# Performance work log

Measured on AMD Instinct MI355X. Metric: run time of the kernel, lower is better.

## Reference

```python
import jax, jax.numpy as jnp
import numpy as np

N_TASK = 100_000
N_DATA = 50_000
E = 1_500_000
D_TASK = 64
D_DATA = 64
D_EDGE = 16
H = 2
C = 64


def setup_inputs() -> dict:
    key = jax.random.key(0)
    ks = jax.random.split(key, 16)
    g = lambda k, shape, s=0.05: jax.random.normal(k, shape, jnp.float32) * s
    return {
        "task_x": jax.random.normal(ks[0], (N_TASK, D_TASK), jnp.float32),
        "data_x": jax.random.normal(ks[1], (N_DATA, D_DATA), jnp.float32),
        "edge_attr": jax.random.normal(ks[2], (E, D_EDGE), jnp.float32),
        "src_idx": jax.random.randint(ks[3], (E,), 0, N_DATA),
        "dst_idx": jax.random.randint(ks[4], (E,), 0, N_TASK),
        # GATv2Conv params
        "W_l": g(ks[5], (D_DATA, H * C)),   # lin_l (source/data)
        "b_l": jnp.zeros((H * C,), jnp.float32),
        "W_r": g(ks[6], (D_TASK, H * C)),   # lin_r (dest/tasks)
        "b_r": jnp.zeros((H * C,), jnp.float32),
        "W_e": g(ks[7], (D_EDGE, H * C)),   # lin_edge (no bias)
        "att": g(ks[8], (H, C)),
        "W_res": g(ks[9], (D_TASK, C)),     # residual lin (no bias)
        "conv_bias": jnp.zeros((C,), jnp.float32),
        # LayerNorm params
        "ln_g": jnp.ones((C,), jnp.float32),
        "ln_b": jnp.zeros((C,), jnp.float32),
    }


def reference(task_x, data_x, edge_attr, src_idx, dst_idx,
              W_l, b_l, W_r, b_r, W_e, att, W_res, conv_bias, ln_g, ln_b):
    n_task = task_x.shape[0]
    x_l = (data_x @ W_l + b_l).reshape(-1, H, C)      # [N_data, H, C]
    x_r = (task_x @ W_r + b_r).reshape(-1, H, C)      # [N_task, H, C]
    e = (edge_attr @ W_e).reshape(-1, H, C)           # [E, H, C]

    # GATv2 attention: leaky_relu(x_i + x_j + e) . att, negative_slope=0.2
    x = jax.nn.leaky_relu(x_l[src_idx] + x_r[dst_idx] + e, 0.2)  # [E, H, C]
    alpha = jnp.einsum("ehc,hc->eh", x, att)                      # [E, H]

    # per-destination-node segment softmax
    m = jax.ops.segment_max(alpha, dst_idx, num_segments=n_task)  # [N_task, H]
    m = jnp.where(jnp.isfinite(m), m, 0.0)  # empty segments -> 0
    a = jnp.exp(alpha - m[dst_idx])
    denom = jax.ops.segment_sum(a, dst_idx, num_segments=n_task)
    a = a / (denom[dst_idx] + 1e-16)                              # [E, H]

    # message = lin_l(x_src), weighted and scatter-summed to destinations
    out = jax.ops.segment_sum(x_l[src_idx] * a[..., None], dst_idx,
                              num_segments=n_task)                # [N_task, H, C]
    out = out.mean(axis=1)                                        # concat=False -> head mean
    out = out + task_x @ W_res + conv_bias                        # residual + bias

    # LayerNorm over channels
    mu = out.mean(-1, keepdims=True)
    var = out.var(-1, keepdims=True)
    out = (out - mu) / jnp.sqrt(var + 1e-5) * ln_g + ln_b

    out = jax.nn.leaky_relu(out, 0.01)
    return jnp.concatenate([out, task_x], axis=-1)                # [N_task, C + D_TASK]
```

## Files before the change

### kernel.cpp

```cpp
#include <hip/hip_runtime.h>
#include <hip/hip_bf16.h>

#define N_TASK 100000
#define N_DATA 50000
#define NE     1500000
#define PAD    48

typedef _Float16 half2v __attribute__((ext_vector_type(2)));
typedef float    f32x4  __attribute__((ext_vector_type(4)));
typedef unsigned u32x2  __attribute__((ext_vector_type(2)));
typedef int      i32x2  __attribute__((ext_vector_type(2)));
typedef int      i32x4  __attribute__((ext_vector_type(4)));

__device__ __forceinline__ unsigned pack_f16(float a, float b) {
    half2v h = {(_Float16)a, (_Float16)b};
    return __builtin_bit_cast(unsigned, h);
}
__device__ __forceinline__ float f16_lo(unsigned u) {
    half2v h = __builtin_bit_cast(half2v, u); return (float)h.x;
}
__device__ __forceinline__ float f16_hi(unsigned u) {
    half2v h = __builtin_bit_cast(half2v, u); return (float)h.y;
}
__device__ __forceinline__ unsigned pkrtz(float a, float b) {
    return __builtin_bit_cast(unsigned, __builtin_amdgcn_cvt_pkrtz(a, b));
}
__device__ __forceinline__ float fdot2f(unsigned a, unsigned b, float c) {
#if __has_builtin(__builtin_amdgcn_fdot2)
    return __builtin_amdgcn_fdot2(__builtin_bit_cast(half2v, a),
                                  __builtin_bit_cast(half2v, b), c, false);
#else
    return c + f16_lo(a) * f16_lo(b) + f16_hi(a) * f16_hi(b);
#endif
}
__device__ __forceinline__ float fdot2h(half2v a, half2v b, float c) {
#if __has_builtin(__builtin_amdgcn_fdot2)
    return __builtin_amdgcn_fdot2(a, b, c, false);
#else
    return c + (float)a.x * (float)b.x + (float)a.y * (float)b.y;
#endif
}

template<int CTRL>
__device__ __forceinline__ float dppadd(float p) {
    int s = __builtin_amdgcn_update_dpp(0, __builtin_bit_cast(int, p),
                                        CTRL, 0xf, 0xf, false);
    return p + __builtin_bit_cast(float, s);
}
__device__ __forceinline__ float half_reduce(float p) {
    p = dppadd<0x121>(p);
    p = dppadd<0x122>(p);
    p = dppadd<0x124>(p);
    p = dppadd<0x128>(p);
    p += __builtin_bit_cast(float,
         __builtin_amdgcn_ds_swizzle(__builtin_bit_cast(int, p), 0x401F));
    return p;
}

__device__ __forceinline__ void gemm_tile64(
    const float* __restrict__ X, const float* __restrict__ W,
    const float* __restrict__ bias, unsigned* __restrict__ Yp,
    int nrows, int tb, float* Xs )
{
    int row0 = tb * 64;
    const float4* X4 = (const float4*)(X + (size_t)row0 * 64);
    float4* Xs4 = (float4*)Xs;
#pragma unroll
    for (int gi = 0; gi < 4; ++gi) {
        int g = threadIdx.x + gi * 256;
        float4 v = {0.f, 0.f, 0.f, 0.f};
        if (row0 + (g >> 4) < nrows) v = X4[g];
        Xs4[g] = v;
    }
    __syncthreads();
    int wv = threadIdx.x >> 6, lane = threadIdx.x & 63;
    const float* Xw = Xs + (wv * 16) * 64;
    float2 bb = *(const float2*)(bias + lane * 2);
    float2 acc[16];
#pragma unroll
    for (int r = 0; r < 16; ++r) acc[r] = bb;
#pragma unroll 4
    for (int k4 = 0; k4 < 16; ++k4) {
        float2 w0 = *(const float2*)(W + (k4 * 4 + 0) * 128 + lane * 2);
        float2 w1 = *(const float2*)(W + (k4 * 4 + 1) * 128 + lane * 2);
        float2 w2 = *(const float2*)(W + (k4 * 4 + 2) * 128 + lane * 2);
        float2 w3 = *(const float2*)(W + (k4 * 4 + 3) * 128 + lane * 2);
#pragma unroll
        for (int r = 0; r < 16; ++r) {
            float4 xv = *(const float4*)(Xw + r * 64 + k4 * 4);
            acc[r].x += xv.x * w0.x + xv.y * w1.x + xv.z * w2.x + xv.w * w3.x;
            acc[r].y += xv.x * w0.y + xv.y * w1.y + xv.z * w2.y + xv.w * w3.y;
        }
    }
#pragma unroll
    for (int r = 0; r < 16; ++r) {
        int row = row0 + wv * 16 + r;
        if (row < nrows)
            __builtin_nontemporal_store(pack_f16(acc[r].x, acc[r].y),
                                        &Yp[(size_t)row * 64 + lane]);
    }
}

__device__ __forceinline__ void gemm_tile64_res(
    const float* __restrict__ X, const float* __restrict__ W,
    const float* __restrict__ bias, unsigned short* __restrict__ Y16,
    int nrows, int tb, float* Xs)
{
    int row0 = tb * 64;
    const float4* X4 = (const float4*)(X + (size_t)row0 * 64);
    float4* Xs4 = (float4*)Xs;
#pragma unroll
    for (int gi = 0; gi < 4; ++gi) {
        int g = threadIdx.x + gi * 256;
        float4 v = {0.f, 0.f, 0.f, 0.f};
        if (row0 + (g >> 4) < nrows) v = X4[g];
        Xs4[g] = v;
    }
    __syncthreads();
    int wv = threadIdx.x >> 6, lane = threadIdx.x & 63;
    const float* Xw = Xs + (wv * 16) * 64;
    float bb = bias[lane];
    float acc[16];
#pragma unroll
    for (int r = 0; r < 16; ++r) acc[r] = bb;
#pragma unroll 4
    for (int k4 = 0; k4 < 16; ++k4) {
        float w0 = W[(k4 * 4 + 0) * 64 + lane];
        float w1 = W[(k4 * 4 + 1) * 64 + lane];
        float w2 = W[(k4 * 4 + 2) * 64 + lane];
        float w3 = W[(k4 * 4 + 3) * 64 + lane];
#pragma unroll
        for (int r = 0; r < 16; ++r) {
            float4 xv = *(const float4*)(Xw + r * 64 + k4 * 4);
            acc[r] += xv.x * w0 + xv.y * w1 + xv.z * w2 + xv.w * w3;
        }
    }
#pragma unroll
    for (int r = 0; r < 16; ++r) {
        int row = row0 + wv * 16 + r;
        if (row < nrows)
            __builtin_nontemporal_store(
                __builtin_bit_cast(unsigned short, (_Float16)acc[r]),
                &Y16[(size_t)row * 64 + lane]);
    }
}

#define GP_XR0   782
#define GP_RES0  2345
#define GP_WP    3908
__global__ __launch_bounds__(256) void gemm_pre(
    const float* __restrict__ data_x, const float* __restrict__ Wl,
    const float* __restrict__ bl,
    const float* __restrict__ task_x, const float* __restrict__ Wr,
    const float* __restrict__ br,
    const float* __restrict__ Wres, const float* __restrict__ convb,
    const float* __restrict__ We,
    unsigned* __restrict__ xlb, unsigned* __restrict__ xrb,
    unsigned short* __restrict__ res16, unsigned* __restrict__ Wp)
{
    __shared__ float Xs[64 * 64];
    int b = blockIdx.x;
    if (b < GP_XR0) {
        gemm_tile64(data_x, Wl, bl, xlb, N_DATA, b, Xs);
    } else if (b < GP_RES0) {
        gemm_tile64(task_x, Wr, br, xrb, N_TASK, b - GP_XR0, Xs);
    } else if (b < GP_WP) {
        gemm_tile64_res(task_x, Wres, convb, res16, N_TASK, b - GP_RES0, Xs);
    } else {
#pragma unroll
        for (int r = 0; r < 4; ++r) {
            int idx = threadIdx.x * 4 + r;
            int kp = idx >> 7, col = idx & 127;
            Wp[idx] = pack_f16(We[(2 * kp) * 128 + col],
                               We[(2 * kp + 1) * 128 + col]);
        }
    }
}

#define CS_SC0   11719
__global__ __launch_bounds__(256) void conv_scatter(
    const float* __restrict__ ea, const int* __restrict__ src,
    const int* __restrict__ dst,
    u32x2* __restrict__ eafu2, int* __restrict__ cnt,
    i32x2* __restrict__ sedge)
{
    int b = blockIdx.x;
    if (b < CS_SC0) {
        int g = b * 256 + threadIdx.x;
#pragma unroll
        for (int h = 0; h < 2; ++h) {
            int idx = g + h * 3000000;
            if (idx < 6000000) {
                f32x4 q = __builtin_nontemporal_load((const f32x4*)ea + idx);
                u32x2 o;
                o.x = pkrtz(q.x, q.y);
                o.y = pkrtz(q.z, q.w);
                __builtin_nontemporal_store(o, eafu2 + idx);
            }
        }
    } else {
        int g = (b - CS_SC0) * 256 + threadIdx.x;
        if (g < NE / 4) {
            i32x4 d = __builtin_nontemporal_load((const i32x4*)dst + g);
            i32x4 s = __builtin_nontemporal_load((const i32x4*)src + g);
            int e = g * 4;
            int p0 = atomicAdd(&cnt[d.x], 1);
            if (p0 < PAD) { i32x2 v = {s.x, e};     sedge[d.x * PAD + p0] = v; }
            int p1 = atomicAdd(&cnt[d.y], 1);
            if (p1 < PAD) { i32x2 v = {s.y, e + 1}; sedge[d.y * PAD + p1] = v; }
            int p2 = atomicAdd(&cnt[d.z], 1);
            if (p2 < PAD) { i32x2 v = {s.z, e + 2}; sedge[d.z * PAD + p2] = v; }
            int p3 = atomicAdd(&cnt[d.w], 1);
            if (p3 < PAD) { i32x2 v = {s.w, e + 3}; sedge[d.w * PAD + p3] = v; }
        }
    }
}

__global__ __launch_bounds__(256) void node_gat(
    const unsigned* __restrict__ xlb, const unsigned* __restrict__ xrb,
    const uint4* __restrict__ eaf, const unsigned* __restrict__ Wp,
    const float* __restrict__ att,
    const int* __restrict__ cntArr, const i32x2* __restrict__ sedge,
    const unsigned short* __restrict__ res16, const float* __restrict__ tx,
    const float* __restrict__ g, const float* __restrict__ beta,
    float* __restrict__ out)
{
    int lane = threadIdx.x & 63;
    int li = lane & 31;
    int n = blockIdx.x * 4 + (threadIdx.x >> 6);
    if (n >= N_TASK) return;

    const uint2* Wp2 = (const uint2*)Wp;
    uint2 wp0 = Wp2[0 * 64 + lane], wp1 = Wp2[1 * 64 + lane];
    uint2 wp2 = Wp2[2 * 64 + lane], wp3 = Wp2[3 * 64 + lane];
    uint2 wp4 = Wp2[4 * 64 + lane], wp5 = Wp2[5 * 64 + lane];
    uint2 wp6 = Wp2[6 * 64 + lane], wp7 = Wp2[7 * 64 + lane];

    half2v xrh = __builtin_bit_cast(half2v, xrb[(unsigned)(n * 64 + lane)]);
    float2 atf = *(const float2*)(att + lane * 2);
    half2v ath = {(_Float16)(atf.x * 1.44269504f), (_Float16)(atf.y * 1.44269504f)};
    const half2v hpt2 = {(_Float16)0.2f, (_Float16)0.2f};

    int base = n * PAD;
    int cnt = __builtin_amdgcn_readfirstlane(cntArr[n]);
    cnt = cnt < PAD ? cnt : PAD;

    half2v acch = {(_Float16)0.f, (_Float16)0.f};
    float den = 0.f;

    auto palpha = [&](unsigned xu, uint4 u0, uint4 u1) -> float {
        float ev0 = 0.f, ev1 = 0.f;
        ev0 = fdot2f(u0.x, wp0.x, ev0); ev1 = fdot2f(u0.x, wp0.y, ev1);
        ev0 = fdot2f(u0.y, wp1.x, ev0); ev1 = fdot2f(u0.y, wp1.y, ev1);
        ev0 = fdot2f(u0.z, wp2.x, ev0); ev1 = fdot2f(u0.z, wp2.y, ev1);
        ev0 = fdot2f(u0.w, wp3.x, ev0); ev1 = fdot2f(u0.w, wp3.y, ev1);
        ev0 = fdot2f(u1.x, wp4.x, ev0); ev1 = fdot2f(u1.x, wp4.y, ev1);
        ev0 = fdot2f(u1.y, wp5.x, ev0); ev1 = fdot2f(u1.y, wp5.y, ev1);
        ev0 = fdot2f(u1.z, wp6.x, ev0); ev1 = fdot2f(u1.z, wp6.y, ev1);
        ev0 = fdot2f(u1.w, wp7.x, ev0); ev1 = fdot2f(u1.w, wp7.y, ev1);
        half2v z = __builtin_bit_cast(half2v, xu) + xrh
                 + __builtin_amdgcn_cvt_pkrtz(ev0, ev1);
        half2v z2 = z * hpt2;
#if __has_builtin(__builtin_elementwise_max)
        half2v lr = __builtin_elementwise_max(z, z2);
#else
        half2v lr; lr.x = z.x > z2.x ? z.x : z2.x; lr.y = z.y > z2.y ? z.y : z2.y;
#endif
        return fdot2h(lr, ath, 0.f);
    };
    auto accum = [&](float w, unsigned xu) {
        _Float16 wh = (_Float16)w;
        half2v w2 = {wh, wh};
        acch = acch + w2 * __builtin_bit_cast(half2v, xu);
        den += w;
    };

#define PAYLOAD(se, xu, e0, e1) do {                                         \
    int s_ = __builtin_amdgcn_readfirstlane((se).x);                         \
    int e_ = __builtin_amdgcn_readfirstlane((se).y);                         \
    xu = xlb[(unsigned)(s_ * 64 + lane)];                                    \
    const uint4* p_ = eaf + (unsigned)(e_ * 2);                              \
    e0 = p_[0]; e1 = p_[1];                                                  \
} while (0)

    i32x2 se0 = {0, 0}, se1 = {0, 0};
    unsigned xuA = 0, xuB = 0;
    uint4 A0 = {0,0,0,0}, A1 = {0,0,0,0}, B0 = {0,0,0,0}, B1 = {0,0,0,0};
    if (cnt > 0) se0 = sedge[base];
    if (cnt > 1) se1 = sedge[base + 1];
    if (cnt > 0) PAYLOAD(se0, xuA, A0, A1);
    if (cnt > 1) PAYLOAD(se1, xuB, B0, B1);
    if (cnt > 2) se0 = sedge[base + 2];
    if (cnt > 3) se1 = sedge[base + 3];

    int i = 0;
    for (; i + 2 <= cnt; i += 2) {
        float pA = palpha(xuA, A0, A1);
        float pB = palpha(xuB, B0, B1);
        unsigned cA = xuA, cB = xuB;
        if (i + 2 < cnt) PAYLOAD(se0, xuA, A0, A1);
        if (i + 3 < cnt) PAYLOAD(se1, xuB, B0, B1);
        if (i + 4 < cnt) se0 = sedge[base + i + 4];
        if (i + 5 < cnt) se1 = sedge[base + i + 5];
        pA = half_reduce(pA);
        pB = half_reduce(pB);
        accum(__builtin_amdgcn_exp2f(pA), cA);
        accum(__builtin_amdgcn_exp2f(pB), cB);
    }
    if (i < cnt) {
        float p = half_reduce(palpha(xuA, A0, A1));
        accum(__builtin_amdgcn_exp2f(p), xuA);
    }
#undef PAYLOAD

    float inv = 1.f / (den + 1e-16f);
    float o0 = (float)acch.x * inv, o1 = (float)acch.y * inv;

    float m0 = 0.5f * (o0 + __shfl_xor(o0, 32));
    float m1 = 0.5f * (o1 + __shfl_xor(o1, 32));

    unsigned ru = ((const unsigned*)res16)[(unsigned)(n * 32 + li)];
    float o0f = m0 + f16_lo(ru);
    float o1f = m1 + f16_hi(ru);

    float sum = o0f + o1f, ssq = o0f * o0f + o1f * o1f;
    sum = half_reduce(sum);
    ssq = half_reduce(ssq);
    float mu = sum * (1.f / 64.f);
    float var = ssq * (1.f / 64.f) - mu * mu;
    float is = rsqrtf(var + 1e-5f);
    float2 g2 = *(const float2*)(g + li * 2);
    float2 b2 = *(const float2*)(beta + li * 2);
    float x0o = (o0f - mu) * is * g2.x + b2.x;
    float x1o = (o1f - mu) * is * g2.y + b2.y;
    x0o = x0o > 0.f ? x0o : 0.01f * x0o;
    x1o = x1o > 0.f ? x1o : 0.01f * x1o;

    if (lane < 32) {
        float2 o = {x0o, x1o};
        *(float2*)(out + (size_t)n * 128 + li * 2) = o;
    } else {
        float2 t2 = *(const float2*)(tx + (size_t)n * 64 + li * 2);
        *(float2*)(out + (size_t)n * 128 + 64 + li * 2) = t2;
    }
}

extern "C" void kernel_launch(void* const* d_in, const int* in_sizes, int n_in,
                              void* d_out, int out_size, void* d_ws, size_t ws_size,
                              hipStream_t stream)
{
    const float* task_x    = (const float*)d_in[0];
    const float* data_x    = (const float*)d_in[1];
    const float* edge_attr = (const float*)d_in[2];
    const int*   src_idx   = (const int*)d_in[3];
    const int*   dst_idx   = (const int*)d_in[4];
    const float* W_l       = (const float*)d_in[5];
    const float* b_l       = (const float*)d_in[6];
    const float* W_r       = (const float*)d_in[7];
    const float* b_r       = (const float*)d_in[8];
    const float* W_e       = (const float*)d_in[9];
    const float* att       = (const float*)d_in[10];
    const float* W_res     = (const float*)d_in[11];
    const float* conv_bias = (const float*)d_in[12];
    const float* ln_g      = (const float*)d_in[13];
    const float* ln_b      = (const float*)d_in[14];
    float* out = (float*)d_out;

    unsigned* xlb   = (unsigned*)d_ws;
    unsigned* xrb   = xlb + 3200000;
    u32x2*    eaf   = (u32x2*)(xrb + 6400000);
    unsigned short* res16 = (unsigned short*)(eaf + 6000000);
    unsigned* Wp    = (unsigned*)(res16 + 6400000);
    int*      cnt   = (int*)(Wp + 1024);
    i32x2*    sedge = (i32x2*)(cnt + 100000);

    (void)hipMemsetAsync(cnt, 0, 100000 * sizeof(int), stream);
    gemm_pre    <<<3909, 256, 0, stream>>>(data_x, W_l, b_l, task_x, W_r, b_r,
                                           W_res, conv_bias, W_e,
                                           xlb, xrb, res16, Wp);
    conv_scatter<<<13184, 256, 0, stream>>>(edge_attr, src_idx, dst_idx,
                                            eaf, cnt, sedge);
    node_gat    <<<25000, 256, 0, stream>>>(xlb, xrb, (const uint4*)eaf, Wp, att,
                                            cnt, sedge,
                                            res16, task_x, ln_g, ln_b, out);
}
```

Before: 369.7 us.

## Use persistent grid-stride loop with prefetch in edge conversion and scatter kernel

Replaces the 13k-block launch that split edge-attr conversion and CSR scatter across separate blocks with 1465 persistent blocks. Each thread converts 16 strided chunks with a one-ahead software prefetch, then does its share of the atomic scatter. Scatter writes become nontemporal stores. This cuts launch/block overhead and overlaps the scatter with the conversion traffic, but lowers how many loads are in flight at once.

```diff
diff --git a/kernel.cpp b/kernel.cpp
--- a/kernel.cpp
+++ b/kernel.cpp
@@ -177,42 +177,45 @@
     }
 }
 
-#define CS_SC0   11719
+#define SC_T (1465 * 256)
 __global__ __launch_bounds__(256) void conv_scatter(
     const float* __restrict__ ea, const int* __restrict__ src,
     const int* __restrict__ dst,
     u32x2* __restrict__ eafu2, int* __restrict__ cnt,
     i32x2* __restrict__ sedge)
 {
-    int b = blockIdx.x;
-    if (b < CS_SC0) {
-        int g = b * 256 + threadIdx.x;
-#pragma unroll
-        for (int h = 0; h < 2; ++h) {
-            int idx = g + h * 3000000;
-            if (idx < 6000000) {
-                f32x4 q = __builtin_nontemporal_load((const f32x4*)ea + idx);
-                u32x2 o;
-                o.x = pkrtz(q.x, q.y);
-                o.y = pkrtz(q.z, q.w);
-                __builtin_nontemporal_store(o, eafu2 + idx);
-            }
+    int g = blockIdx.x * 256 + threadIdx.x;
+    f32x4 q = __builtin_nontemporal_load((const f32x4*)ea + g);
+#pragma unroll 1
+    for (int h = 0; h < 16; ++h) {
+        int idx = g + h * SC_T;
+        f32x4 cur = q;
+        int nidx = idx + SC_T;
+        if (h + 1 < 16 && nidx < 6000000)
+            q = __builtin_nontemporal_load((const f32x4*)ea + nidx);
+        if (idx < 6000000) {
+            u32x2 o;
+            o.x = pkrtz(cur.x, cur.y);
+            o.y = pkrtz(cur.z, cur.w);
+            __builtin_nontemporal_store(o, eafu2 + idx);
         }
-    } else {
-        int g = (b - CS_SC0) * 256 + threadIdx.x;
-        if (g < NE / 4) {
-            i32x4 d = __builtin_nontemporal_load((const i32x4*)dst + g);
-            i32x4 s = __builtin_nontemporal_load((const i32x4*)src + g);
-            int e = g * 4;
-            int p0 = atomicAdd(&cnt[d.x], 1);
-            if (p0 < PAD) { i32x2 v = {s.x, e};     sedge[d.x * PAD + p0] = v; }
-            int p1 = atomicAdd(&cnt[d.y], 1);
-            if (p1 < PAD) { i32x2 v = {s.y, e + 1}; sedge[d.y * PAD + p1] = v; }
-            int p2 = atomicAdd(&cnt[d.z], 1);
-            if (p2 < PAD) { i32x2 v = {s.z, e + 2}; sedge[d.z * PAD + p2] = v; }
-            int p3 = atomicAdd(&cnt[d.w], 1);
-            if (p3 < PAD) { i32x2 v = {s.w, e + 3}; sedge[d.w * PAD + p3] = v; }
-        }
+    }
+    if (g < NE / 4) {
+        i32x4 d = __builtin_nontemporal_load((const i32x4*)dst + g);
+        i32x4 s = __builtin_nontemporal_load((const i32x4*)src + g);
+        int e = g * 4;
+        int p0 = atomicAdd(&cnt[d.x], 1);
+        if (p0 < PAD) { i32x2 v = {s.x, e};
+            __builtin_nontemporal_store(v, &sedge[d.x * PAD + p0]); }
+        int p1 = atomicAdd(&cnt[d.y], 1);
+        if (p1 < PAD) { i32x2 v = {s.y, e + 1};
+            __builtin_nontemporal_store(v, &sedge[d.y * PAD + p1]); }
+        int p2 = atomicAdd(&cnt[d.z], 1);
+        if (p2 < PAD) { i32x2 v = {s.z, e + 2};
+            __builtin_nontemporal_store(v, &sedge[d.z * PAD + p2]); }
+        int p3 = atomicAdd(&cnt[d.w], 1);
+        if (p3 < PAD) { i32x2 v = {s.w, e + 3};
+            __builtin_nontemporal_store(v, &sedge[d.w * PAD + p3]); }
     }
 }
 
@@ -378,8 +381,8 @@
     gemm_pre    <<<3909, 256, 0, stream>>>(data_x, W_l, b_l, task_x, W_r, b_r,
                                            W_res, conv_bias, W_e,
                                            xlb, xrb, res16, Wp);
-    conv_scatter<<<13184, 256, 0, stream>>>(edge_attr, src_idx, dst_idx,
-                                            eaf, cnt, sedge);
+    conv_scatter<<<1465, 256, 0, stream>>>(edge_attr, src_idx, dst_idx,
+                                           eaf, cnt, sedge);
     node_gat    <<<25000, 256, 0, stream>>>(xlb, xrb, (const uint4*)eaf, Wp, att,
                                             cnt, sedge,
                                             res16, task_x, ln_g, ln_b, out);
```

New measurement: 384.1 us. +3.9%, slower.
